# Optimization experiments

Hardware: AMD Instinct MI355X
Metric: run time of the kernel (lower is better)

The kernel has to match this reference:

```python
import jax, jax.numpy as jnp
import numpy as np

D_MODEL = 1024
N_HEADS = 16
D_K = D_MODEL // N_HEADS


def setup_inputs() -> dict:
    key = jax.random.key(0)
    kx, kq, kk, kv, ko = jax.random.split(key, 5)
    s = 1.0 / np.sqrt(D_MODEL)
    return {
        "x": jax.random.normal(kx, (4, 2048, D_MODEL), dtype=jnp.float32),
        "W_q": jax.random.normal(kq, (D_MODEL, D_MODEL), dtype=jnp.float32) * s,
        "W_k": jax.random.normal(kk, (D_MODEL, D_MODEL), dtype=jnp.float32) * s,
        "W_v": jax.random.normal(kv, (D_MODEL, D_MODEL), dtype=jnp.float32) * s,
        "W_o": jax.random.normal(ko, (D_MODEL, D_MODEL), dtype=jnp.float32) * s,
    }


def reference(x, W_q, W_k, W_v, W_o):
    B, S, _ = x.shape
    # torch nn.Linear computes x @ W.T; our W_* stored as [out, in]-equivalent square,
    # use plain x @ W (equivalent parameterization for a random weight).
    def split_heads(t):  # [B,S,D] -> [B,H,S,d_k]
        return t.reshape(B, S, N_HEADS, D_K).transpose(0, 2, 1, 3)

    Q = split_heads(x @ W_q)
    K = split_heads(x @ W_k)
    V = split_heads(x @ W_v)
    scale = 1.0 / np.sqrt(D_K).astype(np.float32)
    scores = jnp.einsum('bhqd,bhkd->bhqk', Q, K) * scale  # [B,H,S,S]
    causal_mask = jnp.tril(jnp.ones((S, S), dtype=bool))  # True = keep
    scores = jnp.where(causal_mask, scores, jnp.float32(-jnp.inf))
    attn = jax.nn.softmax(scores, axis=-1)
    out = jnp.einsum('bhqk,bhkd->bhqd', attn, V)  # [B,H,S,d_k]
    out = out.transpose(0, 2, 1, 3).reshape(B, S, D_MODEL)
    return out @ W_o
```

## Files before the change

### kernel.cpp

```cpp
#include <hip/hip_runtime.h>
#include <hip/hip_bf16.h>
#include <stdint.h>

#define B_SZ 4
#define SEQ 2048
#define DM 1024
#define NH 16
#define DK 64
#define BH (B_SZ * NH)
#define M_TOT (B_SZ * SEQ)

typedef unsigned short u16;
typedef u16 u16x8 __attribute__((ext_vector_type(8)));
typedef __bf16 bf16x8 __attribute__((ext_vector_type(8)));
typedef float f32x4 __attribute__((ext_vector_type(4)));

__device__ __forceinline__ u16 f2bf(float f) {
    union { float f; uint32_t u; } v; v.f = f;
    uint32_t u = v.u;
    return (u16)((u + 0x7FFFu + ((u >> 16) & 1u)) >> 16);
}

__device__ __forceinline__ u16 f2bf_trunc(float f) {
    union { float f; uint32_t u; } v; v.f = f;
    return (u16)(v.u >> 16);
}

__device__ __forceinline__ f32x4 mfma16(u16x8 a, u16x8 b, f32x4 c) {
    return __builtin_amdgcn_mfma_f32_16x16x32_bf16(
        __builtin_bit_cast(bf16x8, a), __builtin_bit_cast(bf16x8, b), c, 0, 0, 0);
}

__device__ __forceinline__ void gload16_lds(const void* g, void* l) {
    __builtin_amdgcn_global_load_lds(
        (const __attribute__((address_space(1))) void*)(uintptr_t)g,
        (__attribute__((address_space(3))) void*)(uintptr_t)l, 16, 0, 0);
}

__global__ void cvt_bf16_kernel(const float* __restrict__ in, u16* __restrict__ out, int n4) {
    int i = blockIdx.x * blockDim.x + threadIdx.x;
    if (i < n4) {
        float4 v = ((const float4*)in)[i];
        ushort4 o;
        o.x = f2bf(v.x); o.y = f2bf(v.y); o.z = f2bf(v.z); o.w = f2bf(v.w);
        ((ushort4*)out)[i] = o;
    }
}

__global__ void transpose_w_kernel(const float* __restrict__ W0, const float* __restrict__ W1,
                                   u16* __restrict__ Wt) {
    __shared__ u16 tile[32][33];
    int bx = blockIdx.x, by = blockIdx.y, z = blockIdx.z;
    const float* W = z ? W1 : W0;
    u16* Wd = Wt + (size_t)z * DM * DM;
    int t = threadIdx.x;
    for (int i = 0; i < 4; i++) {
        int idx = t + i * 256;
        int r = idx >> 5, c = idx & 31;
        tile[r][c] = f2bf(W[(by * 32 + r) * DM + bx * 32 + c]);
    }
    __syncthreads();
    for (int i = 0; i < 4; i++) {
        int idx = t + i * 256;
        int r2 = idx >> 5, c2 = idx & 31;
        Wd[(bx * 32 + r2) * DM + by * 32 + c2] = tile[c2][r2];
    }
}

template <int AFP32, int MODE>
__global__ __launch_bounds__(256, 2) void gemm128(
    const void* __restrict__ Ain, const u16* __restrict__ Bt,
    void* __restrict__ C0p, void* __restrict__ C1p, float scale0) {
    __shared__ u16 As[128][32];
    __shared__ u16 Bs[128][32];
    const int K = DM;
    int m0 = blockIdx.x * 128;
    int n0 = blockIdx.y * 128;
    int tid = threadIdx.x;
    int lane = tid & 63, wave = tid >> 6;
    int quad = lane >> 4, l15 = lane & 15;
    int wm = wave >> 1, wn = wave & 1;

    f32x4 acc[4][4];
    for (int i = 0; i < 4; i++)
        for (int j = 0; j < 4; j++) acc[i][j] = f32x4{0.f, 0.f, 0.f, 0.f};

    int rS = lane >> 2;
    int cS = (lane & 3) * 8;

    for (int k0 = 0; k0 < K; k0 += 32) {
        __syncthreads();
        if (AFP32) {
            const float* A = (const float*)Ain;
            for (int i = 0; i < 4; i++) {
                int idx = tid + i * 256;
                int r = idx >> 3, c = (idx & 7) * 4;
                float4 v = *(const float4*)(&A[(size_t)(m0 + r) * K + k0 + c]);
                ushort4 o;
                o.x = f2bf(v.x); o.y = f2bf(v.y); o.z = f2bf(v.z); o.w = f2bf(v.w);
                *(ushort4*)(&As[r][c]) = o;
            }
        } else {
            const u16* A = (const u16*)Ain;
            const u16* ga = &A[(size_t)(m0 + wave * 32 + rS) * K + k0 + cS];
            gload16_lds(ga, &As[wave * 32][0]);
            gload16_lds(ga + (size_t)16 * K, &As[wave * 32 + 16][0]);
        }
        {
            const u16* gb = &Bt[(size_t)(n0 + wave * 32 + rS) * K + k0 + cS];
            gload16_lds(gb, &Bs[wave * 32][0]);
            gload16_lds(gb + (size_t)16 * K, &Bs[wave * 32 + 16][0]);
        }
        __syncthreads();
        u16x8 af[4], bfv[4];
        for (int mt = 0; mt < 4; mt++)
            af[mt] = *(const u16x8*)(&As[wm * 64 + mt * 16 + l15][quad * 8]);
        for (int nt = 0; nt < 4; nt++)
            bfv[nt] = *(const u16x8*)(&Bs[wn * 64 + nt * 16 + l15][quad * 8]);
        for (int mt = 0; mt < 4; mt++)
            for (int nt = 0; nt < 4; nt++)
                acc[mt][nt] = mfma16(af[mt], bfv[nt], acc[mt][nt]);
    }

    for (int mt = 0; mt < 4; mt++)
        for (int nt = 0; nt < 4; nt++)
            for (int r = 0; r < 4; r++) {
                int m = m0 + wm * 64 + mt * 16 + quad * 4 + r;
                int n = n0 + wn * 64 + nt * 16 + l15;
                float v = acc[mt][nt][r];
                if (MODE == 0) {
                    v *= (n < 1024) ? scale0 : 1.0f;
                    u16* C = (n < 1024) ? (u16*)C0p : (u16*)C1p;
                    int ne = n & 1023;
                    int b = m >> 11, s = m & 2047;
                    int h = ne >> 6, d = ne & 63;
                    C[(((size_t)(b * NH + h) * SEQ) + s) * DK + d] = f2bf(v);
                } else if (MODE == 1) {
                    ((float*)C0p)[(size_t)m * DM + n] = v;
                } else {
                    int b = m >> 11, s = m & 2047;
                    int h = n >> 6, d = n & 63;
                    ((u16*)C0p)[(((size_t)(b * NH + h) * DK) + d) * SEQ + s] = f2bf(v);
                }
            }
}

__global__ __launch_bounds__(256, 3) void attn_kernel(
    const u16* __restrict__ Qb, const u16* __restrict__ Kb,
    const u16* __restrict__ Vtb, u16* __restrict__ AOb) {
    __shared__ u16 Kl[2][64][64];
    __shared__ u16 Vl[2][64][64];
    __shared__ u16 Pl[64][68];

    int bh = blockIdx.x;
    int qs = 31 - blockIdx.y;
    int q0 = qs * 64;
    int tid = threadIdx.x, lane = tid & 63, wave = tid >> 6;
    int quad = lane >> 4, l15 = lane & 15;
    int b = bh >> 4, h = bh & 15;

    const u16* Qg = Qb + (size_t)bh * SEQ * DK;
    const u16* Kg = Kb + (size_t)bh * SEQ * DK;
    const u16* Vg = Vtb + (size_t)bh * DK * SEQ;

    int rw = lane >> 3;
    int gsw = (lane & 7) ^ rw;
    int sw8 = l15 & 15 & 7;
    u16* Pw = &Pl[wave * 16][0];

    u16x8 aq[2];
    for (int kc = 0; kc < 2; kc++)
        aq[kc] = *(const u16x8*)(
            &Qg[(size_t)(q0 + wave * 16 + l15) * DK + kc * 32 + quad * 8]);

    float lsum[4];
    f32x4 O[4];
    for (int r = 0; r < 4; r++) lsum[r] = 0.f;
    for (int nt = 0; nt < 4; nt++) O[nt] = f32x4{0.f, 0.f, 0.f, 0.f};

    {
        const u16* gk = &Kg[(size_t)(wave * 16 + rw) * DK + gsw * 8];
        gload16_lds(gk, &Kl[0][wave * 16][0]);
        gload16_lds(gk + 8 * DK, &Kl[0][wave * 16 + 8][0]);
        const u16* gv = &Vg[(size_t)(wave * 16 + rw) * SEQ + gsw * 8];
        gload16_lds(gv, &Vl[0][wave * 16][0]);
        gload16_lds(gv + 8 * SEQ, &Vl[0][wave * 16 + 8][0]);
    }
    __syncthreads();

    int buf = 0;
    for (int kt = 0; kt <= qs; kt++) {
        if (kt < qs) {
            int k0n = (kt + 1) * 64;
            const u16* gk = &Kg[(size_t)(k0n + wave * 16 + rw) * DK + gsw * 8];
            gload16_lds(gk, &Kl[buf ^ 1][wave * 16][0]);
            gload16_lds(gk + 8 * DK, &Kl[buf ^ 1][wave * 16 + 8][0]);
            const u16* gv = &Vg[(size_t)(wave * 16 + rw) * SEQ + k0n + gsw * 8];
            gload16_lds(gv, &Vl[buf ^ 1][wave * 16][0]);
            gload16_lds(gv + 8 * SEQ, &Vl[buf ^ 1][wave * 16 + 8][0]);
        }

        f32x4 sc[4];
        for (int nt = 0; nt < 4; nt++) {
            const u16* kr = &Kl[buf][nt * 16 + l15][0];
            u16x8 b0 = *(const u16x8*)(kr + (quad ^ sw8) * 8);
            u16x8 b1 = *(const u16x8*)(kr + ((4 + quad) ^ sw8) * 8);
            f32x4 z = f32x4{0.f, 0.f, 0.f, 0.f};
            z = mfma16(aq[0], b0, z);
            z = mfma16(aq[1], b1, z);
            sc[nt] = z;
        }
        if (kt == qs) {
            for (int nt = 0; nt < 4; nt++)
                for (int r = 0; r < 4; r++) {
                    int qq = wave * 16 + quad * 4 + r;
                    int kk = nt * 16 + l15;
                    float e = exp2f(sc[nt][r]);
                    float pv = (kk <= qq) ? e : 0.f;
                    sc[nt][r] = pv;
                    lsum[r] += pv;
                }
        } else {
            for (int nt = 0; nt < 4; nt++)
                for (int r = 0; r < 4; r++) {
                    float pv = exp2f(sc[nt][r]);
                    sc[nt][r] = pv;
                    lsum[r] += pv;
                }
        }
        for (int nt = 0; nt < 4; nt++)
            for (int r = 0; r < 4; r++)
                Pw[(size_t)(quad * 4 + r) * 68 + nt * 16 + l15] = f2bf_trunc(sc[nt][r]);
        u16x8 ap0 = *(const u16x8*)(&Pw[(size_t)l15 * 68 + quad * 8]);
        u16x8 ap1 = *(const u16x8*)(&Pw[(size_t)l15 * 68 + 32 + quad * 8]);
        for (int nt = 0; nt < 4; nt++) {
            const u16* vr = &Vl[buf][nt * 16 + l15][0];
            u16x8 b0 = *(const u16x8*)(vr + (quad ^ sw8) * 8);
            u16x8 b1 = *(const u16x8*)(vr + ((4 + quad) ^ sw8) * 8);
            O[nt] = mfma16(ap0, b0, O[nt]);
            O[nt] = mfma16(ap1, b1, O[nt]);
        }
        __syncthreads();
        buf ^= 1;
    }

    for (int r = 0; r < 4; r++) {
        float s = lsum[r];
        for (int off = 1; off < 16; off <<= 1) s += __shfl_xor(s, off, 64);
        float inv = 1.0f / s;
        int q = q0 + wave * 16 + quad * 4 + r;
        for (int nt = 0; nt < 4; nt++) {
            int d = nt * 16 + l15;
            AOb[((size_t)(b * SEQ + q)) * DM + h * DK + d] = f2bf(O[nt][r] * inv);
        }
    }
}

extern "C" void kernel_launch(void* const* d_in, const int* in_sizes, int n_in,
                              void* d_out, int out_size, void* d_ws, size_t ws_size,
                              hipStream_t stream) {
    const float* x = (const float*)d_in[0];
    const float* Wq = (const float*)d_in[1];
    const float* Wk = (const float*)d_in[2];
    const float* Wv = (const float*)d_in[3];
    const float* Wo = (const float*)d_in[4];
    float* out = (float*)d_out;

    const size_t HALF = (size_t)M_TOT * DM * 2;
    char* S0 = (char*)d_ws;
    char* S1 = (char*)d_ws + HALF;
    char* D0 = (char*)d_out;
    char* D1 = (char*)d_out + HALF;

    u16* xb  = (u16*)S0;
    u16* Qb  = (u16*)S1;
    u16* Kb  = (u16*)D1;
    u16* Vt  = (u16*)D0;
    u16* AOb = (u16*)S0;
    u16* wqk = (u16*)D0;
    u16* wvt = (u16*)S0;
    u16* wot = (u16*)S1;

    const float cscale = 0.125f * 1.44269504088896f;
    dim3 tg2(32, 32, 2);
    dim3 tg1(32, 32, 1);
    dim3 gg(M_TOT / 128, DM / 128);

    int n4 = M_TOT * DM / 4;
    cvt_bf16_kernel<<<n4 / 256, 256, 0, stream>>>(x, xb, n4);

    transpose_w_kernel<<<tg2, 256, 0, stream>>>(Wq, Wk, wqk);
    dim3 gqk(M_TOT / 128, 2048 / 128);
    gemm128<0, 0><<<gqk, 256, 0, stream>>>(xb, wqk, (void*)Qb, (void*)Kb, cscale);

    transpose_w_kernel<<<tg1, 256, 0, stream>>>(Wv, Wv, wvt);
    gemm128<1, 2><<<gg, 256, 0, stream>>>(x, wvt, (void*)Vt, (void*)Vt, 1.0f);

    dim3 ag(BH, 32);
    attn_kernel<<<ag, 256, 0, stream>>>(Qb, Kb, Vt, AOb);

    transpose_w_kernel<<<tg1, 256, 0, stream>>>(Wo, Wo, wot);
    gemm128<0, 1><<<gg, 256, 0, stream>>>(AOb, wot, (void*)out, (void*)out, 1.0f);
}
```

Before: 291.5 us.

## Enlarge attention query tile to 128 rows so each K/V tile serves two row groups

Each attention block now covers 128 query rows instead of 64, with every wave owning two 16-row groups, so each K/V tile loaded into LDS feeds twice as many MFMAs and global K/V traffic is halved. The P scratch buffer switches from padded rows to an XOR-swizzled layout, and s_setprio hints are placed around the MFMA phases. In exchange the grid has half as many blocks and register use per thread rises. Waves whose causal range is shorter stay idle on the final tile.

Result: faster. 266.9 us (-8.5%).

```diff
diff --git a/kernel.cpp b/kernel.cpp
--- a/kernel.cpp
+++ b/kernel.cpp
@@ -150,11 +150,11 @@
     const u16* __restrict__ Vtb, u16* __restrict__ AOb) {
     __shared__ u16 Kl[2][64][64];
     __shared__ u16 Vl[2][64][64];
-    __shared__ u16 Pl[64][68];
+    __shared__ u16 Pl[4][32][64];
 
     int bh = blockIdx.x;
-    int qs = 31 - blockIdx.y;
-    int q0 = qs * 64;
+    int qs = 15 - blockIdx.y;
+    int q0 = qs * 128;
     int tid = threadIdx.x, lane = tid & 63, wave = tid >> 6;
     int quad = lane >> 4, l15 = lane & 15;
     int b = bh >> 4, h = bh & 15;
@@ -165,18 +165,21 @@
 
     int rw = lane >> 3;
     int gsw = (lane & 7) ^ rw;
-    int sw8 = l15 & 15 & 7;
-    u16* Pw = &Pl[wave * 16][0];
-
-    u16x8 aq[2];
-    for (int kc = 0; kc < 2; kc++)
-        aq[kc] = *(const u16x8*)(
-            &Qg[(size_t)(q0 + wave * 16 + l15) * DK + kc * 32 + quad * 8]);
-
-    float lsum[4];
-    f32x4 O[4];
-    for (int r = 0; r < 4; r++) lsum[r] = 0.f;
-    for (int nt = 0; nt < 4; nt++) O[nt] = f32x4{0.f, 0.f, 0.f, 0.f};
+    int sw8 = l15 & 7;
+    u16* Pw = &Pl[wave][0][0];
+
+    u16x8 aq[2][2];
+    for (int g = 0; g < 2; g++)
+        for (int kc = 0; kc < 2; kc++)
+            aq[g][kc] = *(const u16x8*)(
+                &Qg[(size_t)(q0 + wave * 32 + g * 16 + l15) * DK + kc * 32 + quad * 8]);
+
+    float lsum[2][4];
+    f32x4 O[2][4];
+    for (int g = 0; g < 2; g++)
+        for (int r = 0; r < 4; r++) lsum[g][r] = 0.f;
+    for (int g = 0; g < 2; g++)
+        for (int nt = 0; nt < 4; nt++) O[g][nt] = f32x4{0.f, 0.f, 0.f, 0.f};
 
     {
         const u16* gk = &Kg[(size_t)(wave * 16 + rw) * DK + gsw * 8];
@@ -188,9 +191,11 @@
     }
     __syncthreads();
 
+    int nkt = 2 * qs + 2;
+    int lastkt = 2 * qs + (wave >> 1);
     int buf = 0;
-    for (int kt = 0; kt <= qs; kt++) {
-        if (kt < qs) {
+    for (int kt = 0; kt < nkt; kt++) {
+        if (kt + 1 < nkt) {
             int k0n = (kt + 1) * 64;
             const u16* gk = &Kg[(size_t)(k0n + wave * 16 + rw) * DK + gsw * 8];
             gload16_lds(gk, &Kl[buf ^ 1][wave * 16][0]);
@@ -200,60 +205,97 @@
             gload16_lds(gv + 8 * SEQ, &Vl[buf ^ 1][wave * 16 + 8][0]);
         }
 
-        f32x4 sc[4];
-        for (int nt = 0; nt < 4; nt++) {
-            const u16* kr = &Kl[buf][nt * 16 + l15][0];
-            u16x8 b0 = *(const u16x8*)(kr + (quad ^ sw8) * 8);
-            u16x8 b1 = *(const u16x8*)(kr + ((4 + quad) ^ sw8) * 8);
-            f32x4 z = f32x4{0.f, 0.f, 0.f, 0.f};
-            z = mfma16(aq[0], b0, z);
-            z = mfma16(aq[1], b1, z);
-            sc[nt] = z;
-        }
-        if (kt == qs) {
-            for (int nt = 0; nt < 4; nt++)
-                for (int r = 0; r < 4; r++) {
-                    int qq = wave * 16 + quad * 4 + r;
-                    int kk = nt * 16 + l15;
-                    float e = exp2f(sc[nt][r]);
-                    float pv = (kk <= qq) ? e : 0.f;
-                    sc[nt][r] = pv;
-                    lsum[r] += pv;
+        if (kt <= lastkt) {
+            bool diag = (kt == lastkt);
+            f32x4 sc[2][4];
+            __builtin_amdgcn_s_setprio(1);
+            #pragma unroll
+            for (int nt = 0; nt < 4; nt++) {
+                const u16* kr = &Kl[buf][nt * 16 + l15][0];
+                u16x8 b0 = *(const u16x8*)(kr + (quad ^ sw8) * 8);
+                u16x8 b1 = *(const u16x8*)(kr + ((4 + quad) ^ sw8) * 8);
+                #pragma unroll
+                for (int g = 0; g < 2; g++) {
+                    f32x4 z = f32x4{0.f, 0.f, 0.f, 0.f};
+                    z = mfma16(aq[g][0], b0, z);
+                    z = mfma16(aq[g][1], b1, z);
+                    sc[g][nt] = z;
                 }
-        } else {
-            for (int nt = 0; nt < 4; nt++)
-                for (int r = 0; r < 4; r++) {
-                    float pv = exp2f(sc[nt][r]);
-                    sc[nt][r] = pv;
-                    lsum[r] += pv;
+            }
+            __builtin_amdgcn_s_setprio(0);
+            #pragma unroll
+            for (int g = 0; g < 2; g++) {
+                if (diag) {
+                    #pragma unroll
+                    for (int nt = 0; nt < 4; nt++)
+                        #pragma unroll
+                        for (int r = 0; r < 4; r++) {
+                            int qq = q0 + wave * 32 + g * 16 + quad * 4 + r;
+                            int kk = kt * 64 + nt * 16 + l15;
+                            float e = exp2f(sc[g][nt][r]);
+                            float pv = (kk <= qq) ? e : 0.f;
+                            sc[g][nt][r] = pv;
+                            lsum[g][r] += pv;
+                        }
+                } else {
+                    #pragma unroll
+                    for (int nt = 0; nt < 4; nt++)
+                        #pragma unroll
+                        for (int r = 0; r < 4; r++) {
+                            float pv = exp2f(sc[g][nt][r]);
+                            sc[g][nt][r] = pv;
+                            lsum[g][r] += pv;
+                        }
                 }
-        }
-        for (int nt = 0; nt < 4; nt++)
-            for (int r = 0; r < 4; r++)
-                Pw[(size_t)(quad * 4 + r) * 68 + nt * 16 + l15] = f2bf_trunc(sc[nt][r]);
-        u16x8 ap0 = *(const u16x8*)(&Pw[(size_t)l15 * 68 + quad * 8]);
-        u16x8 ap1 = *(const u16x8*)(&Pw[(size_t)l15 * 68 + 32 + quad * 8]);
-        for (int nt = 0; nt < 4; nt++) {
-            const u16* vr = &Vl[buf][nt * 16 + l15][0];
-            u16x8 b0 = *(const u16x8*)(vr + (quad ^ sw8) * 8);
-            u16x8 b1 = *(const u16x8*)(vr + ((4 + quad) ^ sw8) * 8);
-            O[nt] = mfma16(ap0, b0, O[nt]);
-            O[nt] = mfma16(ap1, b1, O[nt]);
+                #pragma unroll
+                for (int nt = 0; nt < 4; nt++)
+                    #pragma unroll
+                    for (int r = 0; r < 4; r++) {
+                        int prow = g * 16 + quad * 4 + r;
+                        int pcol = nt * 16 + l15;
+                        int scol = (((pcol >> 3) ^ (prow & 7)) << 3) | (pcol & 7);
+                        Pw[prow * 64 + scol] = f2bf_trunc(sc[g][nt][r]);
+                    }
+            }
+            u16x8 ap[2][2];
+            #pragma unroll
+            for (int g = 0; g < 2; g++)
+                #pragma unroll
+                for (int kc = 0; kc < 2; kc++)
+                    ap[g][kc] = *(const u16x8*)(
+                        &Pw[(g * 16 + l15) * 64 + (((kc * 4 + quad) ^ sw8) << 3)]);
+            __builtin_amdgcn_s_setprio(1);
+            #pragma unroll
+            for (int nt = 0; nt < 4; nt++) {
+                const u16* vr = &Vl[buf][nt * 16 + l15][0];
+                u16x8 b0 = *(const u16x8*)(vr + (quad ^ sw8) * 8);
+                u16x8 b1 = *(const u16x8*)(vr + ((4 + quad) ^ sw8) * 8);
+                #pragma unroll
+                for (int g = 0; g < 2; g++) {
+                    O[g][nt] = mfma16(ap[g][0], b0, O[g][nt]);
+                    O[g][nt] = mfma16(ap[g][1], b1, O[g][nt]);
+                }
+            }
+            __builtin_amdgcn_s_setprio(0);
         }
         __syncthreads();
         buf ^= 1;
     }
 
-    for (int r = 0; r < 4; r++) {
-        float s = lsum[r];
-        for (int off = 1; off < 16; off <<= 1) s += __shfl_xor(s, off, 64);
-        float inv = 1.0f / s;
-        int q = q0 + wave * 16 + quad * 4 + r;
-        for (int nt = 0; nt < 4; nt++) {
-            int d = nt * 16 + l15;
-            AOb[((size_t)(b * SEQ + q)) * DM + h * DK + d] = f2bf(O[nt][r] * inv);
-        }
-    }
+    #pragma unroll
+    for (int g = 0; g < 2; g++)
+        #pragma unroll
+        for (int r = 0; r < 4; r++) {
+            float s = lsum[g][r];
+            for (int off = 1; off < 16; off <<= 1) s += __shfl_xor(s, off, 64);
+            float inv = 1.0f / s;
+            int q = q0 + wave * 32 + g * 16 + quad * 4 + r;
+            #pragma unroll
+            for (int nt = 0; nt < 4; nt++) {
+                int d = nt * 16 + l15;
+                AOb[((size_t)(b * SEQ + q)) * DM + h * DK + d] = f2bf(O[g][nt][r] * inv);
+            }
+        }
 }
 
 extern "C" void kernel_launch(void* const* d_in, const int* in_sizes, int n_in,
@@ -296,7 +338,7 @@
     transpose_w_kernel<<<tg1, 256, 0, stream>>>(Wv, Wv, wvt);
     gemm128<1, 2><<<gg, 256, 0, stream>>>(x, wvt, (void*)Vt, (void*)Vt, 1.0f);
 
-    dim3 ag(BH, 32);
+    dim3 ag(BH, 16);
     attn_kernel<<<ag, 256, 0, stream>>>(Qb, Kb, Vt, AOb);
 
     transpose_w_kernel<<<tg1, 256, 0, stream>>>(Wo, Wo, wot);
```
